# Performance work log

Hardware: AMD Instinct MI355X
Metric: run time of the kernel (lower is better)

The kernel has to match this reference:

```python
import jax, jax.numpy as jnp
import numpy as np
import math

W = 256
H = 256
N = 1000
C = 1  # grayscale
ALPHA_MAX = 0.999


def _logit(p):
    return jnp.log(p) - jnp.log1p(-p)


def setup_inputs() -> dict:
    key = jax.random.key(0)
    k0, k1, k2, k3, k4 = jax.random.split(key, 5)
    means = jax.random.uniform(k0, (N, 2), dtype=jnp.float32) * W
    scales = jax.random.uniform(k1, (N, 2), dtype=jnp.float32) * 10.0 + 1.0
    quats = jax.random.uniform(k2, (N,), dtype=jnp.float32) * (2.0 * math.pi)  # rotation angle
    rgbs = _logit(jax.random.uniform(k3, (N, C), dtype=jnp.float32) * 0.3 + 0.1)
    opacities = _logit(jax.random.uniform(k4, (N,), dtype=jnp.float32) * 0.5 + 0.1)
    return {"means": means, "quats": quats, "scales": scales, "rgbs": rgbs, "opacities": opacities}


def _render(means, quats, scales, rgbs, opacities):
    # 2D covariance: Sigma = R diag(s^2) R^T, R = [[c,-s],[s,c]]
    c = jnp.cos(quats)
    s = jnp.sin(quats)
    sx2 = scales[:, 0] ** 2
    sy2 = scales[:, 1] ** 2
    a11 = c * c * sx2 + s * s * sy2
    a12 = c * s * (sx2 - sy2)
    a22 = s * s * sx2 + c * c * sy2
    det = a11 * a22 - a12 * a12
    ia = (a22 / det)[:, None, None]   # Sigma^-1 entries, broadcast over pixels
    ib = (-a12 / det)[:, None, None]
    ic = (a11 / det)[:, None, None]

    xs = jnp.arange(W, dtype=jnp.float32) + 0.5
    ys = jnp.arange(H, dtype=jnp.float32) + 0.5
    X = xs[None, :]   # [1, W] -> broadcasts to [H, W]
    Y = ys[:, None]   # [H, 1]

    dx = X[None] - means[:, 0, None, None]  # [N, H, W] (via broadcast)
    dy = Y[None] - means[:, 1, None, None]
    q = ia * dx * dx + 2.0 * ib * dx * dy + ic * dy * dy  # Mahalanobis^2, [N,H,W]

    opac = jax.nn.sigmoid(opacities)[:, None, None]
    alpha = jnp.minimum(opac * jnp.exp(-0.5 * q), ALPHA_MAX)  # [N,H,W]

    # Front-to-back compositing in index order: T_i = prod_{j<i} (1 - alpha_j)
    log_one_minus = jnp.log1p(-alpha)
    logT = jnp.cumsum(log_one_minus, axis=0) - log_one_minus  # exclusive cumsum
    weights = alpha * jnp.exp(logT)  # [N,H,W]

    colors = jax.nn.sigmoid(rgbs)  # [N,C]
    img = jnp.einsum('nhw,nc->chw', weights, colors)  # [C,H,W]
    return img[None]  # [1,C,H,W]


def reference(means, quats, scales, rgbs, opacities):
    return _render(means, quats, scales, rgbs, opacities)
```

## Files before the change

### kernel.cpp

```cpp
#include <hip/hip_runtime.h>
#include <math.h>

#define IW 256
#define IH 256
#define NG 1000
#define CHUNK 256
#define TILE_W 16
#define TILE_H 16
#define TILES_X (IW / TILE_W)
#define TILES_Y (IH / TILE_H)
#define ALPHA_MAX 0.999f
#define LOG2_EPS -19.93157f
#define LN2 0.6931471805599453f
#define INV_LN2 1.4426950408889634f

__global__ __launch_bounds__(256) void splat2d_kernel(
    const float* __restrict__ means,
    const float* __restrict__ quats,
    const float* __restrict__ scales,
    const float* __restrict__ rgbs,
    const float* __restrict__ opacities,
    float* __restrict__ out)
{
    __shared__ float4 s0[CHUNK];
    __shared__ float4 s1[CHUNK];
    __shared__ int wave_cnt[4];

    const int tid = threadIdx.x;
    const int tx0 = blockIdx.x * TILE_W;
    const int ty0 = blockIdx.y * TILE_H;

    const float midx = (float)tx0 + 0.5f * (TILE_W - 1) + 0.5f;
    const float midy = (float)ty0 + 0.5f * (TILE_H - 1) + 0.5f;
    const float hx = 0.5f * (TILE_W - 1);
    const float hy = 0.5f * (TILE_H - 1);

    const float px = (float)(tx0 + (tid & (TILE_W - 1))) + 0.5f;
    const float py = (float)(ty0 + (tid >> 4)) + 0.5f;

    const int lane = tid & 63;
    const int w    = tid >> 6;

    float T = 1.0f;
    float accum = 0.0f;

    for (int c0 = 0; c0 < NG; c0 += CHUNK) {
        bool keep = false;
        float cx, cy, A, B, Cc, lop, col;
        const int n = c0 + tid;
        if (n < NG) {
            float2 mu = ((const float2*)means)[n];
            float2 sc = ((const float2*)scales)[n];
            float q   = quats[n];
            float opa = opacities[n];
            float rgb = rgbs[n];

            float sq, cq;
            __sincosf(q, &sq, &cq);
            float sx2 = sc.x * sc.x, sy2 = sc.y * sc.y;
            float a11 = cq * cq * sx2 + sq * sq * sy2;
            float a12 = cq * sq * (sx2 - sy2);
            float a22 = sq * sq * sx2 + cq * cq * sy2;
            float det = a11 * a22 - a12 * a12;
            float inv = INV_LN2 / det;
            A   = -0.5f * a22 * inv;
            B   =          a12 * inv;
            Cc  = -0.5f * a11 * inv;
            float op = 1.0f / (1.0f + __expf(-opa));
            lop = __log2f(op);
            col = 1.0f / (1.0f + __expf(-rgb));
            cx = mu.x; cy = mu.y;

            float t  = fmaxf((lop - LOG2_EPS) * LN2, 0.0f);
            float rx = sqrtf(2.0f * a11 * t);
            float ry = sqrtf(2.0f * a22 * t);

            keep = (fabsf(cx - midx) <= hx + rx) &&
                   (fabsf(cy - midy) <= hy + ry);
        }

        __syncthreads();
        unsigned long long m = __ballot(keep);
        int rank = __popcll(m & ((1ull << lane) - 1ull));
        if (lane == 0) wave_cnt[w] = __popcll(m);
        __syncthreads();
        int c0w = wave_cnt[0], c1w = wave_cnt[1], c2w = wave_cnt[2], c3w = wave_cnt[3];
        int off = (w > 0 ? c0w : 0) + (w > 1 ? c1w : 0) + (w > 2 ? c2w : 0);
        const int cnt = c0w + c1w + c2w + c3w;
        if (keep) {
            s0[off + rank] = make_float4(cx, cy, A, B);
            s1[off + rank] = make_float4(Cc, lop, col, 0.0f);
        }
        __syncthreads();

        for (int k = 0; k < cnt; ++k) {
            float4 q0 = s0[k];
            float4 q1 = s1[k];
            float dx = px - q0.x;
            float dy = py - q0.y;
            float t  = fmaf(q0.w, dy, q0.z * dx);
            float e  = fmaf(t, dx, fmaf(q1.x * dy, dy, q1.y));
            float alpha = fminf(__builtin_amdgcn_exp2f(e), ALPHA_MAX);
            accum = fmaf(alpha * T, q1.z, accum);
            T = fmaf(-alpha, T, T);
            if (((k & 7) == 7) && __all(T < 1e-5f)) break;
        }
    }

    const int pix = (ty0 + (tid >> 4)) * IW + tx0 + (tid & (TILE_W - 1));
    out[pix] = accum;
}

extern "C" void kernel_launch(void* const* d_in, const int* in_sizes, int n_in,
                              void* d_out, int out_size, void* d_ws, size_t ws_size,
                              hipStream_t stream) {
    const float* means     = (const float*)d_in[0];
    const float* quats     = (const float*)d_in[1];
    const float* scales    = (const float*)d_in[2];
    const float* rgbs      = (const float*)d_in[3];
    const float* opacities = (const float*)d_in[4];
    float* out = (float*)d_out;

    splat2d_kernel<<<dim3(TILES_X, TILES_Y), 256, 0, stream>>>(
        means, quats, scales, rgbs, opacities, out);
}
```

Measured before the change: 77.82 us.

## Split gaussian list across waves per tile and combine segments associatively

```diff
diff --git a/kernel.cpp b/kernel.cpp
--- a/kernel.cpp
+++ b/kernel.cpp
@@ -4,9 +4,10 @@
 #define IW 256
 #define IH 256
 #define NG 1000
-#define CHUNK 256
+#define NSEG 4
+#define SEG (NG / NSEG)
 #define TILE_W 16
-#define TILE_H 16
+#define TILE_H 4
 #define TILES_X (IW / TILE_W)
 #define TILES_Y (IH / TILE_H)
 #define ALPHA_MAX 0.999f
@@ -22,33 +23,30 @@
     const float* __restrict__ opacities,
     float* __restrict__ out)
 {
-    __shared__ float4 s0[CHUNK];
-    __shared__ float4 s1[CHUNK];
-    __shared__ int wave_cnt[4];
+    __shared__ float4 s0[NSEG][SEG];
+    __shared__ float4 s1[NSEG][SEG];
+    __shared__ float2 comb[64][NSEG];
 
-    const int tid = threadIdx.x;
-    const int tx0 = blockIdx.x * TILE_W;
-    const int ty0 = blockIdx.y * TILE_H;
+    const int tid  = threadIdx.x;
+    const int lane = tid & 63;
+    const int w    = tid >> 6;
+    const int tx0  = blockIdx.x * TILE_W;
+    const int ty0  = blockIdx.y * TILE_H;
 
     const float midx = (float)tx0 + 0.5f * (TILE_W - 1) + 0.5f;
     const float midy = (float)ty0 + 0.5f * (TILE_H - 1) + 0.5f;
     const float hx = 0.5f * (TILE_W - 1);
     const float hy = 0.5f * (TILE_H - 1);
 
-    const float px = (float)(tx0 + (tid & (TILE_W - 1))) + 0.5f;
-    const float py = (float)(ty0 + (tid >> 4)) + 0.5f;
-
-    const int lane = tid & 63;
-    const int w    = tid >> 6;
-
-    float T = 1.0f;
-    float accum = 0.0f;
-
-    for (int c0 = 0; c0 < NG; c0 += CHUNK) {
+    int cnt = 0;
+    const int base = w * SEG;
+    #pragma unroll
+    for (int r = 0; r < 4; ++r) {
+        const int o = r * 64 + lane;
         bool keep = false;
         float cx, cy, A, B, Cc, lop, col;
-        const int n = c0 + tid;
-        if (n < NG) {
+        if (o < SEG) {
+            const int n = base + o;
             float2 mu = ((const float2*)means)[n];
             float2 sc = ((const float2*)scales)[n];
             float q   = quats[n];
@@ -78,37 +76,44 @@
             keep = (fabsf(cx - midx) <= hx + rx) &&
                    (fabsf(cy - midy) <= hy + ry);
         }
-
-        __syncthreads();
         unsigned long long m = __ballot(keep);
         int rank = __popcll(m & ((1ull << lane) - 1ull));
-        if (lane == 0) wave_cnt[w] = __popcll(m);
-        __syncthreads();
-        int c0w = wave_cnt[0], c1w = wave_cnt[1], c2w = wave_cnt[2], c3w = wave_cnt[3];
-        int off = (w > 0 ? c0w : 0) + (w > 1 ? c1w : 0) + (w > 2 ? c2w : 0);
-        const int cnt = c0w + c1w + c2w + c3w;
         if (keep) {
-            s0[off + rank] = make_float4(cx, cy, A, B);
-            s1[off + rank] = make_float4(Cc, lop, col, 0.0f);
+            s0[w][cnt + rank] = make_float4(cx, cy, A, B);
+            s1[w][cnt + rank] = make_float4(Cc, lop, col, 0.0f);
         }
-        __syncthreads();
-
-        for (int k = 0; k < cnt; ++k) {
-            float4 q0 = s0[k];
-            float4 q1 = s1[k];
-            float dx = px - q0.x;
-            float dy = py - q0.y;
-            float t  = fmaf(q0.w, dy, q0.z * dx);
-            float e  = fmaf(t, dx, fmaf(q1.x * dy, dy, q1.y));
-            float alpha = fminf(__builtin_amdgcn_exp2f(e), ALPHA_MAX);
-            accum = fmaf(alpha * T, q1.z, accum);
-            T = fmaf(-alpha, T, T);
-            if (((k & 7) == 7) && __all(T < 1e-5f)) break;
-        }
+        cnt += __popcll(m);
     }
 
-    const int pix = (ty0 + (tid >> 4)) * IW + tx0 + (tid & (TILE_W - 1));
-    out[pix] = accum;
+    const float px = (float)(tx0 + (lane & (TILE_W - 1))) + 0.5f;
+    const float py = (float)(ty0 + (lane >> 4)) + 0.5f;
+
+    float T = 1.0f;
+    float accum = 0.0f;
+    for (int k = 0; k < cnt; ++k) {
+        float4 q0 = s0[w][k];
+        float4 q1 = s1[w][k];
+        float dx = px - q0.x;
+        float dy = py - q0.y;
+        float t  = fmaf(q0.w, dy, q0.z * dx);
+        float e  = fmaf(t, dx, fmaf(q1.x * dy, dy, q1.y));
+        float alpha = fminf(__builtin_amdgcn_exp2f(e), ALPHA_MAX);
+        accum = fmaf(alpha * T, q1.z, accum);
+        T = fmaf(-alpha, T, T);
+    }
+    comb[lane][w] = make_float2(accum, T);
+
+    __syncthreads();
+    if (w == 0) {
+        float c = 0.0f, Tt = 1.0f;
+        #pragma unroll
+        for (int s = 0; s < NSEG; ++s) {
+            float2 v = comb[lane][s];
+            c  = fmaf(Tt, v.x, c);
+            Tt *= v.y;
+        }
+        out[(ty0 + (lane >> 4)) * IW + tx0 + (lane & (TILE_W - 1))] = c;
+    }
 }
 
 extern "C" void kernel_launch(void* const* d_in, const int* in_sizes, int n_in,
```

Result: faster. 67.27 us (-13.6%).
